# Performance work log

Measured on AMD Instinct MI355X. Metric: run time of the kernel, lower is better.

Reference implementation:

```python
import math
import jax, jax.numpy as jnp
import numpy as np

N_USERS = 100000
N_ITEMS = 50000
NNZ = 1600000
BATCH = 64
ORDER = 8
FLATNESS = 2


def cheby_coeffs(order, flatness):
    # plateau target on Chebyshev extrema grid
    x = np.arange(order + 1)
    xv = np.round(np.cos((order - x) / order * math.pi), 3)
    tgt = np.where(xv < 0,
                   np.power(-xv, flatness) * 0.5 + 0.5,
                   np.power(xv, flatness) * (-0.5) + 0.5)
    tgt = np.round(tgt, 3)
    # Chebyshev nodes
    k = np.arange(1, order + 2)
    nodes = np.cos((order + 1 + 0.5 - k) / (order + 1) * math.pi)
    # Chebyshev recurrence evaluated at nodes, scaled by target
    out = [tgt * np.ones_like(nodes) * 0 + tgt, nodes * tgt]
    for _ in range(2, order + 1):
        out.append(nodes * out[-1] * 2 - out[-2])
    c = np.stack(out).sum(axis=1) * (2.0 / (order + 1))
    c[0] /= 2
    return jnp.asarray(c, dtype=jnp.float32)


def setup_inputs() -> dict:
    key = jax.random.key(0)
    k1, k2, k3 = jax.random.split(key, 3)
    signal = jax.random.normal(k1, (BATCH, N_ITEMS), dtype=jnp.float32)
    row = jax.random.randint(k2, (NNZ,), 0, N_USERS)
    col = jax.random.randint(k3, (NNZ,), 0, N_ITEMS)
    # symmetric degree normalization D_u^{-1/2} A D_i^{-1/2}
    du = jnp.bincount(row, length=N_USERS).astype(jnp.float32)
    di = jnp.bincount(col, length=N_ITEMS).astype(jnp.float32)
    du_is = jnp.where(du > 0, jnp.clip(du, 1.0) ** -0.5, 0.0)
    di_is = jnp.where(di > 0, jnp.clip(di, 1.0) ** -0.5, 0.0)
    vals = du_is[row] * di_is[col]
    return {"signal": signal, "vals": vals, "row": row, "col": col}


def reference(signal, vals, row, col):
    coeffs = cheby_coeffs(ORDER, FLATNESS)

    def lap(x):  # x: [n_items, batch];  L*x = x - 2 * A^T (A x)
        y = jax.ops.segment_sum(vals[:, None] * x[col], row, num_segments=N_USERS)
        z = jax.ops.segment_sum(vals[:, None] * y[row], col, num_segments=N_ITEMS)
        return x - 2.0 * z

    s = signal.T  # [n_items, batch]
    t0 = s
    t1 = lap(s)
    out = coeffs[0] * t0 + coeffs[1] * t1
    for k in range(2, ORDER + 1):
        t2 = lap(t1) * 2.0 - t0
        out = out + coeffs[k] * t2
        t0, t1 = t1, t2
    return out.T
```

## Files before the change

### kernel.cpp

```cpp
#include <hip/hip_runtime.h>
#include <hip/hip_fp16.h>
#include <math.h>

#define NUSERS 100000
#define NITEMS 50000
#define BATCH  64
#define ORDER  8
#define BSHIFT 9
#define BROWS  (1 << BSHIFT)
#define NBUCKU ((NUSERS + BROWS - 1) >> BSHIFT)
#define NBUCKI ((NITEMS + BROWS - 1) >> BSHIFT)
#define CAPU 16384
#define CAPI 24576
#define S1_BLOCKS 512
#define NREP 4


struct __align__(8) Half4 { __half2 a, b; };
struct Coeffs { float v[ORDER + 1]; };

#define SLOT ((size_t)(NITEMS + 1) * BATCH)

__device__ __forceinline__ void acc_pk(float4& acc, Half4 v0, Half4 v1,
                                       Half4 v2, Half4 v3) {
    __half2 sa = __hadd2(__hadd2(v0.a, v1.a), __hadd2(v2.a, v3.a));
    __half2 sb = __hadd2(__hadd2(v0.b, v1.b), __hadd2(v2.b, v3.b));
    float2 fa = __half22float2(sa);
    float2 fb = __half22float2(sb);
    acc.x += fa.x; acc.y += fa.y; acc.z += fb.x; acc.w += fb.y;
}

__device__ __forceinline__ Half4 to_h4(float x, float y, float z, float w) {
    Half4 h;
    h.a = __floats2half2_rn(x, y);
    h.b = __floats2half2_rn(z, w);
    return h;
}

__global__ void init_bcur(int* __restrict__ bcurU, int* __restrict__ bcurI) {
    int t = blockIdx.x * blockDim.x + threadIdx.x;
    if (t < NBUCKU) bcurU[t] = t * CAPU;
    if (t < NBUCKI) bcurI[t] = t * CAPI;
}

__global__ void zero_pads(__half* __restrict__ tauHall, __half* __restrict__ ybuf) {
    int t = threadIdx.x;
    for (int k = 0; k <= ORDER; ++k)
        if (t < BATCH) tauHall[(size_t)k * SLOT + (size_t)NITEMS * BATCH + t] = __float2half(0.f);
    if (t < BATCH) ybuf[(size_t)NUSERS * BATCH + t] = __float2half(0.f);
}

__global__ void scatter1(const int* __restrict__ row, const int* __restrict__ col,
                         int* __restrict__ bcurU, int* __restrict__ bcurI,
                         int* __restrict__ stU, int* __restrict__ stI, int nnz) {
    __shared__ int cU[NREP][NBUCKU];
    __shared__ int cI[NREP][NBUCKI];
    const int chunk = (nnz + S1_BLOCKS - 1) / S1_BLOCKS;
    const int b0 = blockIdx.x * chunk;
    const int e0 = min(b0 + chunk, nnz);
    const int sw = threadIdx.x >> 6;
    for (int t = threadIdx.x; t < NREP * NBUCKU; t += blockDim.x) (&cU[0][0])[t] = 0;
    for (int t = threadIdx.x; t < NREP * NBUCKI; t += blockDim.x) (&cI[0][0])[t] = 0;
    __syncthreads();
    for (int i = b0 + threadIdx.x; i < e0; i += blockDim.x) {
        atomicAdd(&cU[sw][row[i] >> BSHIFT], 1);
        atomicAdd(&cI[sw][col[i] >> BSHIFT], 1);
    }
    __syncthreads();
    for (int t = threadIdx.x; t < NBUCKU; t += blockDim.x) {
        int c0 = cU[0][t], c1 = cU[1][t], c2 = cU[2][t], c3 = cU[3][t];
        int tot = c0 + c1 + c2 + c3;
        int base = (tot > 0) ? atomicAdd(&bcurU[t], tot) : 0;
        cU[0][t] = base;
        cU[1][t] = base + c0;
        cU[2][t] = base + c0 + c1;
        cU[3][t] = base + c0 + c1 + c2;
    }
    for (int t = threadIdx.x; t < NBUCKI; t += blockDim.x) {
        int c0 = cI[0][t], c1 = cI[1][t], c2 = cI[2][t], c3 = cI[3][t];
        int tot = c0 + c1 + c2 + c3;
        int base = (tot > 0) ? atomicAdd(&bcurI[t], tot) : 0;
        cI[0][t] = base;
        cI[1][t] = base + c0;
        cI[2][t] = base + c0 + c1;
        cI[3][t] = base + c0 + c1 + c2;
    }
    __syncthreads();
    for (int i = b0 + threadIdx.x; i < e0; i += blockDim.x) {
        int r = row[i], c = col[i];
        int pu = atomicAdd(&cU[sw][r >> BSHIFT], 1);
        stU[pu] = ((r & (BROWS - 1)) << 17) | c;
        int pi = atomicAdd(&cI[sw][c >> BSHIFT], 1);
        stI[pi] = ((c & (BROWS - 1)) << 17) | r;
    }
}

__global__ void scatter2(const int* __restrict__ bcur, const int* __restrict__ st,
                         int* __restrict__ ptr, int* __restrict__ degOut,
                         int* __restrict__ outIdx, int nrows, int cap, int dummyIdx) {
    __shared__ int deg[BROWS];
    __shared__ int ps[256];
    __shared__ int cur[BROWS];
    __shared__ int rs[BROWS];
    const int rbase = blockIdx.x << BSHIFT;
    const int nr = min(BROWS, nrows - rbase);
    const int lo = blockIdx.x * cap;
    const int hi = bcur[blockIdx.x];
    const int t = threadIdx.x;
    deg[2 * t] = 0;
    deg[2 * t + 1] = 0;
    __syncthreads();
    for (int j = lo + t; j < hi; j += 256)
        atomicAdd(&deg[st[j] >> 17], 1);
    __syncthreads();
    int a = deg[2 * t];
    int b = deg[2 * t + 1];
    int pa = (a + 15) & ~15;
    int pb = (b + 15) & ~15;
    ps[t] = pa + pb;
    __syncthreads();
    for (int off = 1; off < 256; off <<= 1) {
        int u = (t >= off) ? ps[t - off] : 0;
        __syncthreads();
        ps[t] += u;
        __syncthreads();
    }
    int excl = (t > 0) ? ps[t - 1] : 0;
    int p0 = lo + excl;
    int p1 = p0 + pa;
    rs[2 * t] = p0;
    rs[2 * t + 1] = p1;
    cur[2 * t] = p0;
    cur[2 * t + 1] = p1;
    if (2 * t < nr)     { ptr[rbase + 2 * t] = p0;     degOut[rbase + 2 * t] = a; }
    if (2 * t + 1 < nr) { ptr[rbase + 2 * t + 1] = p1; degOut[rbase + 2 * t + 1] = b; }
    __syncthreads();
    for (int j = lo + t; j < hi; j += 256) {
        int v = st[j];
        int p = atomicAdd(&cur[v >> 17], 1);
        outIdx[p] = v & 0x1FFFF;
    }
    __syncthreads();
    for (int i = t; i < nr; i += 256) {
        int endReal = cur[i];
        int endPad  = rs[i] + ((deg[i] + 15) & ~15);
        for (int j = endReal; j < endPad; ++j) outIdx[j] = dummyIdx;
    }
}

__global__ void transpose_scale_k(const float* __restrict__ in,
                                  const int* __restrict__ ideg,
                                  float* __restrict__ out,
                                  __half* __restrict__ outH) {
    __shared__ float tile[32][33];
    const int cb = blockIdx.x * 32;
    const int rb = blockIdx.y * 32;
    for (int i = threadIdx.y; i < 32; i += 8) {
        int r = rb + i, c = cb + threadIdx.x;
        if (r < BATCH && c < NITEMS) tile[i][threadIdx.x] = in[(size_t)r * NITEMS + c];
    }
    __syncthreads();
    for (int i = threadIdx.y; i < 32; i += 8) {
        int c = cb + i, r = rb + threadIdx.x;
        if (c < NITEMS && r < BATCH) {
            int d = ideg[c];
            float dis = (d > 0) ? rsqrtf((float)d) : 0.0f;
            float v = dis * tile[threadIdx.x][i];
            out[(size_t)c * BATCH + r] = v;
            outH[(size_t)c * BATCH + r] = __float2half(v);
        }
    }
}

__global__ void transpose_out_k(const __half* __restrict__ tauHall,
                                const float* __restrict__ signal,
                                const int* __restrict__ ideg, float csum, Coeffs cf,
                                float* __restrict__ out) {
    __shared__ float tile[32][33];
    const int cb = blockIdx.x * 32;
    const int rb = blockIdx.y * 32;
    for (int i = threadIdx.y; i < 32; i += 8) {
        int r = rb + i, c = cb + threadIdx.x;
        if (r < NITEMS && c < BATCH) {
            size_t base = (size_t)r * BATCH + c;
            float s = 0.f;
            #pragma unroll
            for (int k = 0; k <= ORDER; ++k)
                s += cf.v[k] * __half2float(tauHall[(size_t)k * SLOT + base]);
            tile[i][threadIdx.x] = s;
        }
    }
    __syncthreads();
    for (int i = threadIdx.y; i < 32; i += 8) {
        int c = cb + i, r = rb + threadIdx.x;
        if (c < BATCH && r < NITEMS) {
            int d = ideg[r];
            float v = (d > 0) ? sqrtf((float)d) * tile[threadIdx.x][i]
                              : csum * signal[(size_t)c * NITEMS + r];
            out[(size_t)c * NITEMS + r] = v;
        }
    }
}

__device__ __forceinline__ void gather4_p(const int* __restrict__ idx,
                                          const Half4* __restrict__ x,
                                          const int* b, const int* n,
                                          int sub, int bh, float4* a) {
    const char* __restrict__ xb = (const char*)x;
    const char* __restrict__ ib = (const char*)idx;
    const unsigned bhoff = (unsigned)bh << 3;
    unsigned jb[4];
    int nmax = 0;
    #pragma unroll
    for (int q = 0; q < 4; ++q) {
        jb[q] = ((unsigned)b[q] << 2) + ((unsigned)sub << 4);
        nmax = max(nmax, n[q]);
    }
    for (int it = 0; it < nmax; ++it) {
        #pragma unroll
        for (int q = 0; q < 4; ++q) {
            if (it < n[q]) {
                int4 ii = *(const int4*)(ib + jb[q]);
                Half4 v0 = *(const Half4*)(xb + (((unsigned)ii.x << 7) + bhoff));
                Half4 v1 = *(const Half4*)(xb + (((unsigned)ii.y << 7) + bhoff));
                Half4 v2 = *(const Half4*)(xb + (((unsigned)ii.z << 7) + bhoff));
                Half4 v3 = *(const Half4*)(xb + (((unsigned)ii.w << 7) + bhoff));
                acc_pk(a[q], v0, v1, v2, v3);
                jb[q] += 64;
            }
        }
    }
    #pragma unroll
    for (int q = 0; q < 4; ++q) {
        a[q].x += __shfl_xor(a[q].x, 16); a[q].y += __shfl_xor(a[q].y, 16);
        a[q].z += __shfl_xor(a[q].z, 16); a[q].w += __shfl_xor(a[q].w, 16);
        a[q].x += __shfl_xor(a[q].x, 32); a[q].y += __shfl_xor(a[q].y, 32);
        a[q].z += __shfl_xor(a[q].z, 32); a[q].w += __shfl_xor(a[q].w, 32);
    }
}

__global__ void spmm_user(const int* __restrict__ ptr, const int* __restrict__ deg,
                          const int* __restrict__ idx,
                          const Half4* __restrict__ tauH, Half4* __restrict__ y) {
    const int lane = threadIdx.x & 63;
    const int w = (blockIdx.x * blockDim.x + threadIdx.x) >> 6;
    const int H = NUSERS / 4;
    if (w >= H) return;
    int r[4] = {w, w + H, w + 2 * H, w + 3 * H};
    const int sub = lane >> 4;
    const int bh  = lane & 15;
    int b[4], d[4], n[4];
    #pragma unroll
    for (int q = 0; q < 4; ++q) {
        b[q] = ptr[r[q]];
        d[q] = deg[r[q]];
        n[q] = (d[q] + 15) >> 4;
    }
    float4 a[4] = {{0,0,0,0},{0,0,0,0},{0,0,0,0},{0,0,0,0}};
    gather4_p(idx, tauH, b, n, sub, bh, a);
    if (sub == 0) {
        #pragma unroll
        for (int q = 0; q < 4; ++q) {
            float s = (d[q] > 0) ? 1.0f / (float)d[q] : 0.0f;
            y[(size_t)r[q] * 16 + bh] = to_h4(s * a[q].x, s * a[q].y, s * a[q].z, s * a[q].w);
        }
    }
}

__global__ void spmm_item_first(const int* __restrict__ ptr, const int* __restrict__ deg,
                                const int* __restrict__ idx, const Half4* __restrict__ y,
                                const float* __restrict__ tau0, float* __restrict__ tau1,
                                Half4* __restrict__ tauH1) {
    const int lane = threadIdx.x & 63;
    const int w = (blockIdx.x * blockDim.x + threadIdx.x) >> 6;
    const int H = NITEMS / 4;
    if (w >= H) return;
    int r[4] = {w, w + H, w + 2 * H, w + 3 * H};
    const int sub = lane >> 4;
    const int bh  = lane & 15;
    int b[4], d[4], n[4];
    #pragma unroll
    for (int q = 0; q < 4; ++q) {
        b[q] = ptr[r[q]];
        d[q] = deg[r[q]];
        n[q] = (d[q] + 15) >> 4;
    }
    float4 a[4] = {{0,0,0,0},{0,0,0,0},{0,0,0,0},{0,0,0,0}};
    gather4_p(idx, y, b, n, sub, bh, a);
    if (sub == 0) {
        #pragma unroll
        for (int q = 0; q < 4; ++q) {
            float inv = (d[q] > 0) ? 1.0f / (float)d[q] : 0.0f;
            float s2 = 2.0f * inv;
            size_t base = (size_t)r[q] * BATCH + (bh << 2);
            float4 t0v = *(const float4*)&tau0[base];
            float4 t;
            t.x = t0v.x - s2 * a[q].x; t.y = t0v.y - s2 * a[q].y;
            t.z = t0v.z - s2 * a[q].z; t.w = t0v.w - s2 * a[q].w;
            *(float4*)&tau1[base] = t;
            tauH1[(size_t)r[q] * 16 + bh] = to_h4(t.x, t.y, t.z, t.w);
        }
    }
}

__global__ void spmm_item_k(const int* __restrict__ ptr, const int* __restrict__ deg,
                            const int* __restrict__ idx, const Half4* __restrict__ y,
                            const float* __restrict__ tau1, float* __restrict__ tau0,
                            Half4* __restrict__ tauHk) {
    const int lane = threadIdx.x & 63;
    const int w = (blockIdx.x * blockDim.x + threadIdx.x) >> 6;
    const int H = NITEMS / 4;
    if (w >= H) return;
    int r[4] = {w, w + H, w + 2 * H, w + 3 * H};
    const int sub = lane >> 4;
    const int bh  = lane & 15;
    int b[4], d[4], n[4];
    #pragma unroll
    for (int q = 0; q < 4; ++q) {
        b[q] = ptr[r[q]];
        d[q] = deg[r[q]];
        n[q] = (d[q] + 15) >> 4;
    }
    float4 a[4] = {{0,0,0,0},{0,0,0,0},{0,0,0,0},{0,0,0,0}};
    gather4_p(idx, y, b, n, sub, bh, a);
    if (sub == 0) {
        #pragma unroll
        for (int q = 0; q < 4; ++q) {
            float inv = (d[q] > 0) ? 1.0f / (float)d[q] : 0.0f;
            float s4 = 4.0f * inv;
            size_t base = (size_t)r[q] * BATCH + (bh << 2);
            float4 t1v = *(const float4*)&tau1[base];
            float4 t0v = *(const float4*)&tau0[base];
            float4 t2;
            t2.x = 2.0f * t1v.x - s4 * a[q].x - t0v.x;
            t2.y = 2.0f * t1v.y - s4 * a[q].y - t0v.y;
            t2.z = 2.0f * t1v.z - s4 * a[q].z - t0v.z;
            t2.w = 2.0f * t1v.w - s4 * a[q].w - t0v.w;
            *(float4*)&tau0[base] = t2;
            tauHk[(size_t)r[q] * 16 + bh] = to_h4(t2.x, t2.y, t2.z, t2.w);
        }
    }
}

static void cheby_coeffs_host(float* c) {
    const int order = ORDER, flatness = 2;
    const double PI = 3.14159265358979323846;
    double tgt[ORDER + 1], nodes[ORDER + 1];
    for (int x = 0; x <= order; ++x) {
        double xv = cos((double)(order - x) / order * PI);
        xv = nearbyint(xv * 1000.0) / 1000.0;
        double t = (xv < 0.0) ? pow(-xv, (double)flatness) * 0.5 + 0.5
                              : pow(xv, (double)flatness) * (-0.5) + 0.5;
        tgt[x] = nearbyint(t * 1000.0) / 1000.0;
    }
    for (int k = 1; k <= order + 1; ++k)
        nodes[k - 1] = cos((order + 1 + 0.5 - k) / (double)(order + 1) * PI);

    double prev[ORDER + 1], cur[ORDER + 1], nxt[ORDER + 1];
    double sums[ORDER + 1];
    double s0 = 0, s1 = 0;
    for (int i = 0; i <= order; ++i) {
        prev[i] = tgt[i];
        cur[i]  = nodes[i] * tgt[i];
        s0 += prev[i];
        s1 += cur[i];
    }
    sums[0] = s0; sums[1] = s1;
    for (int j = 2; j <= order; ++j) {
        double s = 0;
        for (int i = 0; i <= order; ++i) {
            nxt[i] = nodes[i] * cur[i] * 2.0 - prev[i];
            s += nxt[i];
        }
        sums[j] = s;
        for (int i = 0; i <= order; ++i) { prev[i] = cur[i]; cur[i] = nxt[i]; }
    }
    for (int j = 0; j <= order; ++j)
        c[j] = (float)(sums[j] * (2.0 / (order + 1)));
    c[0] *= 0.5f;
}

extern "C" void kernel_launch(void* const* d_in, const int* in_sizes, int n_in,
                              void* d_out, int out_size, void* d_ws, size_t ws_size,
                              hipStream_t stream) {
    const float* signal = (const float*)d_in[0];
    const int*   row    = (const int*)d_in[2];
    const int*   col    = (const int*)d_in[3];
    const int nnz = in_sizes[1];

    char* wsb = (char*)d_ws;
    size_t off = 0;
    auto carve = [&](size_t nbytes) {
        void* p = wsb + off;
        off += (nbytes + 255) & ~(size_t)255;
        return p;
    };
    const size_t NB = (size_t)NITEMS * BATCH;
    const size_t NEU = (size_t)NBUCKU * CAPU;
    const size_t NEI = (size_t)NBUCKI * CAPI;
    float*  tauA   = (float*)carve(NB * 4);
    float*  tauB   = (float*)carve(NB * 4);
    __half* tauHall = (__half*)carve((ORDER + 1) * SLOT * 2);
    Half4*  ybuf   = (Half4*)carve(((size_t)NUSERS + 1) * BATCH * 2);
    int*    uptr   = (int*)carve(NUSERS * 4);
    int*    iptr   = (int*)carve(NITEMS * 4);
    int*    udeg   = (int*)carve(NUSERS * 4);
    int*    ideg   = (int*)carve(NITEMS * 4);
    int*    bcurU  = (int*)carve(NBUCKU * 4);
    int*    bcurI  = (int*)carve(NBUCKI * 4);
    int*    ucol   = (int*)carve(NEU * 4);
    int*    irow   = (int*)carve(NEI * 4);
    int*    stU    = (int*)tauHall;
    int*    stI    = (int*)tauHall + NEU;
    (void)ws_size;

    float c[ORDER + 1];
    cheby_coeffs_host(c);
    Coeffs cf;
    float csum = 0.f;
    for (int k = 0; k <= ORDER; ++k) { cf.v[k] = c[k]; csum += c[k]; }

    init_bcur<<<(NBUCKU + 255) / 256, 256, 0, stream>>>(bcurU, bcurI);
    scatter1<<<S1_BLOCKS, 256, 0, stream>>>(row, col, bcurU, bcurI, stU, stI, nnz);
    scatter2<<<NBUCKU, 256, 0, stream>>>(bcurU, stU, uptr, udeg, ucol, NUSERS, CAPU, NITEMS);
    scatter2<<<NBUCKI, 256, 0, stream>>>(bcurI, stI, iptr, ideg, irow, NITEMS, CAPI, NUSERS);
    zero_pads<<<1, 256, 0, stream>>>(tauHall, (__half*)ybuf);

    dim3 tb(32, 8);
    transpose_scale_k<<<dim3((NITEMS + 31) / 32, (BATCH + 31) / 32), tb, 0, stream>>>(
        signal, ideg, tauA, tauHall);

    const int ug = ((NUSERS / 4) * 64 + 255) / 256;
    const int ig = ((NITEMS / 4) * 64 + 255) / 256;

    spmm_user<<<ug, 256, 0, stream>>>(uptr, udeg, ucol, (const Half4*)tauHall, ybuf);
    spmm_item_first<<<ig, 256, 0, stream>>>(iptr, ideg, irow, ybuf, tauA, tauB,
                                            (Half4*)(tauHall + SLOT));

    float* t0 = tauA;
    float* t1 = tauB;
    for (int k = 2; k <= ORDER; ++k) {
        spmm_user<<<ug, 256, 0, stream>>>(uptr, udeg, ucol,
                                          (const Half4*)(tauHall + (size_t)(k - 1) * SLOT), ybuf);
        spmm_item_k<<<ig, 256, 0, stream>>>(iptr, ideg, irow, ybuf, t1, t0,
                                            (Half4*)(tauHall + (size_t)k * SLOT));
        float* tmp = t0; t0 = t1; t1 = tmp;
    }

    transpose_out_k<<<dim3((BATCH + 31) / 32, (NITEMS + 31) / 32), tb, 0, stream>>>(
        tauHall, signal, ideg, csum, cf, (float*)d_out);
}
```

Baseline: 755.2 us.

## Split batch into 16-column chunks to shrink gather working set for cache residency

Processes the 64-column batch in four independent chunks of 16 columns, running the full Chebyshev recurrence per chunk with narrower half2 gathers and per-chunk transpose kernels. Each chunk's dense vectors are a quarter the size, so the randomly gathered item and user rows are more likely to stay in L2/LLC. In exchange, the CSR index arrays are read four times, kernel launches quadruple, and each gathered row is only 32 bytes, which may waste sector bandwidth.

```diff
diff --git a/kernel.cpp b/kernel.cpp
--- a/kernel.cpp
+++ b/kernel.cpp
@@ -5,6 +5,8 @@
 #define NUSERS 100000
 #define NITEMS 50000
 #define BATCH  64
+#define CB     16
+#define NCHUNK (BATCH / CB)
 #define ORDER  8
 #define BSHIFT 9
 #define BROWS  (1 << BSHIFT)
@@ -16,26 +18,9 @@
 #define NREP 4
 
 
-struct __align__(8) Half4 { __half2 a, b; };
 struct Coeffs { float v[ORDER + 1]; };
 
-#define SLOT ((size_t)(NITEMS + 1) * BATCH)
-
-__device__ __forceinline__ void acc_pk(float4& acc, Half4 v0, Half4 v1,
-                                       Half4 v2, Half4 v3) {
-    __half2 sa = __hadd2(__hadd2(v0.a, v1.a), __hadd2(v2.a, v3.a));
-    __half2 sb = __hadd2(__hadd2(v0.b, v1.b), __hadd2(v2.b, v3.b));
-    float2 fa = __half22float2(sa);
-    float2 fb = __half22float2(sb);
-    acc.x += fa.x; acc.y += fa.y; acc.z += fb.x; acc.w += fb.y;
-}
-
-__device__ __forceinline__ Half4 to_h4(float x, float y, float z, float w) {
-    Half4 h;
-    h.a = __floats2half2_rn(x, y);
-    h.b = __floats2half2_rn(z, w);
-    return h;
-}
+#define SLOTC ((size_t)(NITEMS + 1) * CB)
 
 __global__ void init_bcur(int* __restrict__ bcurU, int* __restrict__ bcurI) {
     int t = blockIdx.x * blockDim.x + threadIdx.x;
@@ -45,9 +30,11 @@
 
 __global__ void zero_pads(__half* __restrict__ tauHall, __half* __restrict__ ybuf) {
     int t = threadIdx.x;
-    for (int k = 0; k <= ORDER; ++k)
-        if (t < BATCH) tauHall[(size_t)k * SLOT + (size_t)NITEMS * BATCH + t] = __float2half(0.f);
-    if (t < BATCH) ybuf[(size_t)NUSERS * BATCH + t] = __float2half(0.f);
+    if (t < CB) {
+        for (int k = 0; k <= ORDER; ++k)
+            tauHall[(size_t)k * SLOTC + (size_t)NITEMS * CB + t] = __float2half(0.f);
+        ybuf[(size_t)NUSERS * CB + t] = __float2half(0.f);
+    }
 }
 
 __global__ void scatter1(const int* __restrict__ row, const int* __restrict__ col,
@@ -148,107 +135,110 @@
     }
 }
 
-__global__ void transpose_scale_k(const float* __restrict__ in,
-                                  const int* __restrict__ ideg,
-                                  float* __restrict__ out,
-                                  __half* __restrict__ outH) {
-    __shared__ float tile[32][33];
-    const int cb = blockIdx.x * 32;
-    const int rb = blockIdx.y * 32;
-    for (int i = threadIdx.y; i < 32; i += 8) {
-        int r = rb + i, c = cb + threadIdx.x;
-        if (r < BATCH && c < NITEMS) tile[i][threadIdx.x] = in[(size_t)r * NITEMS + c];
-    }
-    __syncthreads();
-    for (int i = threadIdx.y; i < 32; i += 8) {
-        int c = cb + i, r = rb + threadIdx.x;
-        if (c < NITEMS && r < BATCH) {
-            int d = ideg[c];
-            float dis = (d > 0) ? rsqrtf((float)d) : 0.0f;
-            float v = dis * tile[threadIdx.x][i];
-            out[(size_t)c * BATCH + r] = v;
-            outH[(size_t)c * BATCH + r] = __float2half(v);
-        }
-    }
-}
-
-__global__ void transpose_out_k(const __half* __restrict__ tauHall,
-                                const float* __restrict__ signal,
-                                const int* __restrict__ ideg, float csum, Coeffs cf,
-                                float* __restrict__ out) {
-    __shared__ float tile[32][33];
-    const int cb = blockIdx.x * 32;
-    const int rb = blockIdx.y * 32;
-    for (int i = threadIdx.y; i < 32; i += 8) {
-        int r = rb + i, c = cb + threadIdx.x;
-        if (r < NITEMS && c < BATCH) {
-            size_t base = (size_t)r * BATCH + c;
-            float s = 0.f;
-            #pragma unroll
-            for (int k = 0; k <= ORDER; ++k)
-                s += cf.v[k] * __half2float(tauHall[(size_t)k * SLOT + base]);
-            tile[i][threadIdx.x] = s;
-        }
-    }
-    __syncthreads();
-    for (int i = threadIdx.y; i < 32; i += 8) {
-        int c = cb + i, r = rb + threadIdx.x;
-        if (c < BATCH && r < NITEMS) {
-            int d = ideg[r];
-            float v = (d > 0) ? sqrtf((float)d) * tile[threadIdx.x][i]
-                              : csum * signal[(size_t)c * NITEMS + r];
-            out[(size_t)c * NITEMS + r] = v;
-        }
-    }
-}
-
-__device__ __forceinline__ void gather4_p(const int* __restrict__ idx,
-                                          const Half4* __restrict__ x,
-                                          const int* b, const int* n,
-                                          int sub, int bh, float4* a) {
-    const char* __restrict__ xb = (const char*)x;
+__global__ void transpose_scale_cb(const float* __restrict__ in, int b0,
+                                   const int* __restrict__ ideg,
+                                   float* __restrict__ tauF,
+                                   __half* __restrict__ tauH) {
+    int c = blockIdx.x * blockDim.x + threadIdx.x;
+    if (c >= NITEMS) return;
+    int d = ideg[c];
+    float dis = (d > 0) ? rsqrtf((float)d) : 0.0f;
+    float v[CB];
+    #pragma unroll
+    for (int r = 0; r < CB; ++r)
+        v[r] = dis * in[(size_t)(b0 + r) * NITEMS + c];
+    #pragma unroll
+    for (int r = 0; r < CB; r += 4)
+        *(float4*)&tauF[(size_t)c * CB + r] = make_float4(v[r], v[r+1], v[r+2], v[r+3]);
+    union { __half2 h2[8]; uint4 u4[2]; } pk;
+    #pragma unroll
+    for (int j = 0; j < 8; ++j) pk.h2[j] = __floats2half2_rn(v[2*j], v[2*j+1]);
+    uint4* dst = (uint4*)&tauH[(size_t)c * CB];
+    dst[0] = pk.u4[0];
+    dst[1] = pk.u4[1];
+}
+
+__global__ void transpose_out_cb(const __half* __restrict__ tauHall, int b0,
+                                 const float* __restrict__ signal,
+                                 const int* __restrict__ ideg, float csum, Coeffs cf,
+                                 float* __restrict__ out) {
+    int c = blockIdx.x * blockDim.x + threadIdx.x;
+    if (c >= NITEMS) return;
+    float s[CB];
+    #pragma unroll
+    for (int r = 0; r < CB; ++r) s[r] = 0.f;
+    for (int k = 0; k <= ORDER; ++k) {
+        union { uint4 u4[2]; __half2 h2[8]; } pk;
+        const uint4* src = (const uint4*)&tauHall[(size_t)k * SLOTC + (size_t)c * CB];
+        pk.u4[0] = src[0];
+        pk.u4[1] = src[1];
+        float ck = cf.v[k];
+        #pragma unroll
+        for (int j = 0; j < 8; ++j) {
+            float2 f = __half22float2(pk.h2[j]);
+            s[2*j]     += ck * f.x;
+            s[2*j + 1] += ck * f.y;
+        }
+    }
+    int d = ideg[c];
+    if (d > 0) {
+        float sc = sqrtf((float)d);
+        #pragma unroll
+        for (int r = 0; r < CB; ++r)
+            out[(size_t)(b0 + r) * NITEMS + c] = sc * s[r];
+    } else {
+        #pragma unroll
+        for (int r = 0; r < CB; ++r)
+            out[(size_t)(b0 + r) * NITEMS + c] = csum * signal[(size_t)(b0 + r) * NITEMS + c];
+    }
+}
+
+__device__ __forceinline__ void gather4_cb(const int* __restrict__ idx,
+                                           const __half2* __restrict__ x2,
+                                           const int* b, const int* n,
+                                           int sub, int bh, float2* a) {
+    const char* __restrict__ xb = (const char*)x2;
     const char* __restrict__ ib = (const char*)idx;
-    const unsigned bhoff = (unsigned)bh << 3;
+    const unsigned bhoff = (unsigned)bh << 2;
     unsigned jb[4];
     int nmax = 0;
     #pragma unroll
     for (int q = 0; q < 4; ++q) {
-        jb[q] = ((unsigned)b[q] << 2) + ((unsigned)sub << 4);
+        jb[q] = ((unsigned)b[q] + ((unsigned)sub << 1)) << 2;
         nmax = max(nmax, n[q]);
     }
     for (int it = 0; it < nmax; ++it) {
         #pragma unroll
         for (int q = 0; q < 4; ++q) {
             if (it < n[q]) {
-                int4 ii = *(const int4*)(ib + jb[q]);
-                Half4 v0 = *(const Half4*)(xb + (((unsigned)ii.x << 7) + bhoff));
-                Half4 v1 = *(const Half4*)(xb + (((unsigned)ii.y << 7) + bhoff));
-                Half4 v2 = *(const Half4*)(xb + (((unsigned)ii.z << 7) + bhoff));
-                Half4 v3 = *(const Half4*)(xb + (((unsigned)ii.w << 7) + bhoff));
-                acc_pk(a[q], v0, v1, v2, v3);
+                int2 ii = *(const int2*)(ib + jb[q]);
+                __half2 v0 = *(const __half2*)(xb + (((unsigned)ii.x << 5) + bhoff));
+                __half2 v1 = *(const __half2*)(xb + (((unsigned)ii.y << 5) + bhoff));
+                float2 f = __half22float2(__hadd2(v0, v1));
+                a[q].x += f.x;
+                a[q].y += f.y;
                 jb[q] += 64;
             }
         }
     }
     #pragma unroll
     for (int q = 0; q < 4; ++q) {
+        a[q].x += __shfl_xor(a[q].x, 8);  a[q].y += __shfl_xor(a[q].y, 8);
         a[q].x += __shfl_xor(a[q].x, 16); a[q].y += __shfl_xor(a[q].y, 16);
-        a[q].z += __shfl_xor(a[q].z, 16); a[q].w += __shfl_xor(a[q].w, 16);
         a[q].x += __shfl_xor(a[q].x, 32); a[q].y += __shfl_xor(a[q].y, 32);
-        a[q].z += __shfl_xor(a[q].z, 32); a[q].w += __shfl_xor(a[q].w, 32);
-    }
-}
-
-__global__ void spmm_user(const int* __restrict__ ptr, const int* __restrict__ deg,
-                          const int* __restrict__ idx,
-                          const Half4* __restrict__ tauH, Half4* __restrict__ y) {
+    }
+}
+
+__global__ void spmm_user_cb(const int* __restrict__ ptr, const int* __restrict__ deg,
+                             const int* __restrict__ idx,
+                             const __half2* __restrict__ tauH2, __half2* __restrict__ y2) {
     const int lane = threadIdx.x & 63;
     const int w = (blockIdx.x * blockDim.x + threadIdx.x) >> 6;
     const int H = NUSERS / 4;
     if (w >= H) return;
     int r[4] = {w, w + H, w + 2 * H, w + 3 * H};
-    const int sub = lane >> 4;
-    const int bh  = lane & 15;
+    const int sub = lane >> 3;
+    const int bh  = lane & 7;
     int b[4], d[4], n[4];
     #pragma unroll
     for (int q = 0; q < 4; ++q) {
@@ -256,28 +246,28 @@
         d[q] = deg[r[q]];
         n[q] = (d[q] + 15) >> 4;
     }
-    float4 a[4] = {{0,0,0,0},{0,0,0,0},{0,0,0,0},{0,0,0,0}};
-    gather4_p(idx, tauH, b, n, sub, bh, a);
-    if (sub == 0) {
+    float2 a[4] = {{0,0},{0,0},{0,0},{0,0}};
+    gather4_cb(idx, tauH2, b, n, sub, bh, a);
+    if (lane < 8) {
         #pragma unroll
         for (int q = 0; q < 4; ++q) {
             float s = (d[q] > 0) ? 1.0f / (float)d[q] : 0.0f;
-            y[(size_t)r[q] * 16 + bh] = to_h4(s * a[q].x, s * a[q].y, s * a[q].z, s * a[q].w);
-        }
-    }
-}
-
-__global__ void spmm_item_first(const int* __restrict__ ptr, const int* __restrict__ deg,
-                                const int* __restrict__ idx, const Half4* __restrict__ y,
-                                const float* __restrict__ tau0, float* __restrict__ tau1,
-                                Half4* __restrict__ tauH1) {
+            y2[(size_t)r[q] * 8 + bh] = __floats2half2_rn(s * a[q].x, s * a[q].y);
+        }
+    }
+}
+
+__global__ void spmm_item_first_cb(const int* __restrict__ ptr, const int* __restrict__ deg,
+                                   const int* __restrict__ idx, const __half2* __restrict__ y2,
+                                   const float* __restrict__ tau0, float* __restrict__ tau1,
+                                   __half2* __restrict__ tauH1) {
     const int lane = threadIdx.x & 63;
     const int w = (blockIdx.x * blockDim.x + threadIdx.x) >> 6;
     const int H = NITEMS / 4;
     if (w >= H) return;
     int r[4] = {w, w + H, w + 2 * H, w + 3 * H};
-    const int sub = lane >> 4;
-    const int bh  = lane & 15;
+    const int sub = lane >> 3;
+    const int bh  = lane & 7;
     int b[4], d[4], n[4];
     #pragma unroll
     for (int q = 0; q < 4; ++q) {
@@ -285,35 +275,35 @@
         d[q] = deg[r[q]];
         n[q] = (d[q] + 15) >> 4;
     }
-    float4 a[4] = {{0,0,0,0},{0,0,0,0},{0,0,0,0},{0,0,0,0}};
-    gather4_p(idx, y, b, n, sub, bh, a);
-    if (sub == 0) {
+    float2 a[4] = {{0,0},{0,0},{0,0},{0,0}};
+    gather4_cb(idx, y2, b, n, sub, bh, a);
+    if (lane < 8) {
         #pragma unroll
         for (int q = 0; q < 4; ++q) {
             float inv = (d[q] > 0) ? 1.0f / (float)d[q] : 0.0f;
             float s2 = 2.0f * inv;
-            size_t base = (size_t)r[q] * BATCH + (bh << 2);
-            float4 t0v = *(const float4*)&tau0[base];
-            float4 t;
-            t.x = t0v.x - s2 * a[q].x; t.y = t0v.y - s2 * a[q].y;
-            t.z = t0v.z - s2 * a[q].z; t.w = t0v.w - s2 * a[q].w;
-            *(float4*)&tau1[base] = t;
-            tauH1[(size_t)r[q] * 16 + bh] = to_h4(t.x, t.y, t.z, t.w);
-        }
-    }
-}
-
-__global__ void spmm_item_k(const int* __restrict__ ptr, const int* __restrict__ deg,
-                            const int* __restrict__ idx, const Half4* __restrict__ y,
-                            const float* __restrict__ tau1, float* __restrict__ tau0,
-                            Half4* __restrict__ tauHk) {
+            size_t base = (size_t)r[q] * CB + (bh << 1);
+            float2 t0v = *(const float2*)&tau0[base];
+            float2 t;
+            t.x = t0v.x - s2 * a[q].x;
+            t.y = t0v.y - s2 * a[q].y;
+            *(float2*)&tau1[base] = t;
+            tauH1[(size_t)r[q] * 8 + bh] = __floats2half2_rn(t.x, t.y);
+        }
+    }
+}
+
+__global__ void spmm_item_k_cb(const int* __restrict__ ptr, const int* __restrict__ deg,
+                               const int* __restrict__ idx, const __half2* __restrict__ y2,
+                               const float* __restrict__ tau1, float* __restrict__ tau0,
+                               __half2* __restrict__ tauHk) {
     const int lane = threadIdx.x & 63;
     const int w = (blockIdx.x * blockDim.x + threadIdx.x) >> 6;
     const int H = NITEMS / 4;
     if (w >= H) return;
     int r[4] = {w, w + H, w + 2 * H, w + 3 * H};
-    const int sub = lane >> 4;
-    const int bh  = lane & 15;
+    const int sub = lane >> 3;
+    const int bh  = lane & 7;
     int b[4], d[4], n[4];
     #pragma unroll
     for (int q = 0; q < 4; ++q) {
@@ -321,23 +311,21 @@
         d[q] = deg[r[q]];
         n[q] = (d[q] + 15) >> 4;
     }
-    float4 a[4] = {{0,0,0,0},{0,0,0,0},{0,0,0,0},{0,0,0,0}};
-    gather4_p(idx, y, b, n, sub, bh, a);
-    if (sub == 0) {
+    float2 a[4] = {{0,0},{0,0},{0,0},{0,0}};
+    gather4_cb(idx, y2, b, n, sub, bh, a);
+    if (lane < 8) {
         #pragma unroll
         for (int q = 0; q < 4; ++q) {
             float inv = (d[q] > 0) ? 1.0f / (float)d[q] : 0.0f;
             float s4 = 4.0f * inv;
-            size_t base = (size_t)r[q] * BATCH + (bh << 2);
-            float4 t1v = *(const float4*)&tau1[base];
-            float4 t0v = *(const float4*)&tau0[base];
-            float4 t2;
+            size_t base = (size_t)r[q] * CB + (bh << 1);
+            float2 t1v = *(const float2*)&tau1[base];
+            float2 t0v = *(const float2*)&tau0[base];
+            float2 t2;
             t2.x = 2.0f * t1v.x - s4 * a[q].x - t0v.x;
             t2.y = 2.0f * t1v.y - s4 * a[q].y - t0v.y;
-            t2.z = 2.0f * t1v.z - s4 * a[q].z - t0v.z;
-            t2.w = 2.0f * t1v.w - s4 * a[q].w - t0v.w;
-            *(float4*)&tau0[base] = t2;
-            tauHk[(size_t)r[q] * 16 + bh] = to_h4(t2.x, t2.y, t2.z, t2.w);
+            *(float2*)&tau0[base] = t2;
+            tauHk[(size_t)r[q] * 8 + bh] = __floats2half2_rn(t2.x, t2.y);
         }
     }
 }
@@ -395,13 +383,12 @@
         off += (nbytes + 255) & ~(size_t)255;
         return p;
     };
-    const size_t NB = (size_t)NITEMS * BATCH;
     const size_t NEU = (size_t)NBUCKU * CAPU;
     const size_t NEI = (size_t)NBUCKI * CAPI;
-    float*  tauA   = (float*)carve(NB * 4);
-    float*  tauB   = (float*)carve(NB * 4);
-    __half* tauHall = (__half*)carve((ORDER + 1) * SLOT * 2);
-    Half4*  ybuf   = (Half4*)carve(((size_t)NUSERS + 1) * BATCH * 2);
+    float*  tauFA  = (float*)carve((size_t)NITEMS * CB * 4);
+    float*  tauFB  = (float*)carve((size_t)NITEMS * CB * 4);
+    __half* tauH   = (__half*)carve((ORDER + 1) * SLOTC * 2);
+    __half* ybuf   = (__half*)carve(((size_t)NUSERS + 1) * CB * 2);
     int*    uptr   = (int*)carve(NUSERS * 4);
     int*    iptr   = (int*)carve(NITEMS * 4);
     int*    udeg   = (int*)carve(NUSERS * 4);
@@ -410,8 +397,8 @@
     int*    bcurI  = (int*)carve(NBUCKI * 4);
     int*    ucol   = (int*)carve(NEU * 4);
     int*    irow   = (int*)carve(NEI * 4);
-    int*    stU    = (int*)tauHall;
-    int*    stI    = (int*)tauHall + NEU;
+    int*    stU    = (int*)carve(NEU * 4);
+    int*    stI    = (int*)carve(NEI * 4);
     (void)ws_size;
 
     float c[ORDER + 1];
@@ -420,33 +407,40 @@
     float csum = 0.f;
     for (int k = 0; k <= ORDER; ++k) { cf.v[k] = c[k]; csum += c[k]; }
 
-    init_bcur<<<(NBUCKU + 255) / 256, 256, 0, stream>>>(bcurU, bcurI);
+    init_bcur<<<1, 256, 0, stream>>>(bcurU, bcurI);
     scatter1<<<S1_BLOCKS, 256, 0, stream>>>(row, col, bcurU, bcurI, stU, stI, nnz);
     scatter2<<<NBUCKU, 256, 0, stream>>>(bcurU, stU, uptr, udeg, ucol, NUSERS, CAPU, NITEMS);
     scatter2<<<NBUCKI, 256, 0, stream>>>(bcurI, stI, iptr, ideg, irow, NITEMS, CAPI, NUSERS);
-    zero_pads<<<1, 256, 0, stream>>>(tauHall, (__half*)ybuf);
-
-    dim3 tb(32, 8);
-    transpose_scale_k<<<dim3((NITEMS + 31) / 32, (BATCH + 31) / 32), tb, 0, stream>>>(
-        signal, ideg, tauA, tauHall);
-
-    const int ug = ((NUSERS / 4) * 64 + 255) / 256;
-    const int ig = ((NITEMS / 4) * 64 + 255) / 256;
-
-    spmm_user<<<ug, 256, 0, stream>>>(uptr, udeg, ucol, (const Half4*)tauHall, ybuf);
-    spmm_item_first<<<ig, 256, 0, stream>>>(iptr, ideg, irow, ybuf, tauA, tauB,
-                                            (Half4*)(tauHall + SLOT));
-
-    float* t0 = tauA;
-    float* t1 = tauB;
-    for (int k = 2; k <= ORDER; ++k) {
-        spmm_user<<<ug, 256, 0, stream>>>(uptr, udeg, ucol,
-                                          (const Half4*)(tauHall + (size_t)(k - 1) * SLOT), ybuf);
-        spmm_item_k<<<ig, 256, 0, stream>>>(iptr, ideg, irow, ybuf, t1, t0,
-                                            (Half4*)(tauHall + (size_t)k * SLOT));
-        float* tmp = t0; t0 = t1; t1 = tmp;
-    }
-
-    transpose_out_k<<<dim3((BATCH + 31) / 32, (NITEMS + 31) / 32), tb, 0, stream>>>(
-        tauHall, signal, ideg, csum, cf, (float*)d_out);
-}
+    zero_pads<<<1, 64, 0, stream>>>(tauH, ybuf);
+
+    const int ug = (NUSERS / 4) * 64 / 256;
+    const int ig = (NITEMS / 4) * 64 / 256;
+    const int tg = (NITEMS + 255) / 256;
+
+    for (int ch = 0; ch < NCHUNK; ++ch) {
+        const int b0 = ch * CB;
+
+        transpose_scale_cb<<<tg, 256, 0, stream>>>(signal, b0, ideg, tauFA, tauH);
+
+        spmm_user_cb<<<ug, 256, 0, stream>>>(uptr, udeg, ucol,
+                                             (const __half2*)tauH, (__half2*)ybuf);
+        spmm_item_first_cb<<<ig, 256, 0, stream>>>(iptr, ideg, irow,
+                                                   (const __half2*)ybuf, tauFA, tauFB,
+                                                   (__half2*)(tauH + SLOTC));
+
+        float* t0 = tauFA;
+        float* t1 = tauFB;
+        for (int k = 2; k <= ORDER; ++k) {
+            spmm_user_cb<<<ug, 256, 0, stream>>>(uptr, udeg, ucol,
+                                                 (const __half2*)(tauH + (size_t)(k - 1) * SLOTC),
+                                                 (__half2*)ybuf);
+            spmm_item_k_cb<<<ig, 256, 0, stream>>>(iptr, ideg, irow,
+                                                   (const __half2*)ybuf, t1, t0,
+                                                   (__half2*)(tauH + (size_t)k * SLOTC));
+            float* tmp = t0; t0 = t1; t1 = tmp;
+        }
+
+        transpose_out_cb<<<tg, 256, 0, stream>>>(tauH, b0, signal, ideg, csum, cf,
+                                                 (float*)d_out);
+    }
+}
```

Measured after the change: 1.664 ms. +120.4%, slower.
